# Kernel tuning notes

Measured on AMD Instinct MI355X. Metric: run time of the kernel, lower is better.

The kernel has to match this reference:

```python
import jax, jax.numpy as jnp
import numpy as np

N_NODES = 100000
N_EDGES = 1600000
IN_FEATS = 128
H_FEATS = 64
NEG_SLOPE = 0.2


def gat_layer(x, W, a_l, a_r, b, src, dst):
    # x: [N, Fin], W: [Fin, Fout], a_l/a_r/b: [Fout]
    h = x @ W                                   # [N, Fout]
    el = h @ a_l                                # [N]
    er = h @ a_r                                # [N]
    e = el[src] + er[dst]                       # [E]
    e = jnp.where(e > 0, e, NEG_SLOPE * e)      # leaky_relu
    # segment softmax over incoming edges of each dst node
    m = jax.ops.segment_max(e, dst, num_segments=N_NODES)   # [N], -inf for deg-0
    ex = jnp.exp(e - m[dst])                                 # [E]
    s = jax.ops.segment_sum(ex, dst, num_segments=N_NODES)   # [N]
    alpha = ex / s[dst]                                      # [E]
    out = jax.ops.segment_sum(alpha[:, None] * h[src], dst, num_segments=N_NODES)
    return jax.nn.relu(out + b)


def setup_inputs() -> dict:
    key = jax.random.key(0)
    ks = jax.random.split(key, 16)
    in_feat = jax.random.normal(ks[0], (N_NODES, IN_FEATS), dtype=jnp.float32)
    src = jax.random.randint(ks[1], (N_EDGES,), 0, N_NODES, dtype=jnp.int32)
    dst = jax.random.randint(ks[2], (N_EDGES,), 0, N_NODES, dtype=jnp.int32)
    def w(k, fin, fout):
        return jax.random.normal(k, (fin, fout), dtype=jnp.float32) * (1.0 / np.sqrt(fin))
    def v(k, f):
        return jax.random.normal(k, (f,), dtype=jnp.float32) * 0.1
    return {
        "in_feat": in_feat, "src": src, "dst": dst,
        "W1": w(ks[3], IN_FEATS, H_FEATS), "al1": v(ks[4], H_FEATS), "ar1": v(ks[5], H_FEATS), "b1": jnp.zeros((H_FEATS,), jnp.float32),
        "W2": w(ks[6], H_FEATS, H_FEATS), "al2": v(ks[7], H_FEATS), "ar2": v(ks[8], H_FEATS), "b2": jnp.zeros((H_FEATS,), jnp.float32),
        "W3": w(ks[9], H_FEATS, H_FEATS), "al3": v(ks[10], H_FEATS), "ar3": v(ks[11], H_FEATS), "b3": jnp.zeros((H_FEATS,), jnp.float32),
    }


def reference(in_feat, src, dst, W1, al1, ar1, b1, W2, al2, ar2, b2, W3, al3, ar3, b3):
    h = gat_layer(in_feat, W1, al1, ar1, b1, src, dst)
    h = gat_layer(h, W2, al2, ar2, b2, src, dst)
    h = gat_layer(h, W3, al3, ar3, b3, src, dst)
    return h
```

## Files before the change

### kernel.cpp

```cpp
#include <hip/hip_runtime.h>
#include <hip/hip_fp16.h>
#include <math.h>

#define HF 64
#define LEAKY 0.2f
#define NBLK 256
#define NPB 512
#define MAXNB 256

typedef _Float16 f16x2 __attribute__((ext_vector_type(2)));

__device__ __forceinline__ float dot2f(f16x2 a, f16x2 b, float c) {
#if __has_builtin(__builtin_amdgcn_fdot2)
    return __builtin_amdgcn_fdot2(a, b, c, false);
#else
    return fmaf((float)a[0], (float)b[0], fmaf((float)a[1], (float)b[1], c));
#endif
}


__global__ __launch_bounds__(256)
void part_count(const int* __restrict__ dst, int* __restrict__ Cmat, int E, int nb) {
    __shared__ int lc[MAXNB];
    int tid = threadIdx.x;
    for (int t = tid; t < nb; t += 256) lc[t] = 0;
    __syncthreads();
    int chunk = (E + NBLK - 1) / NBLK;
    int b0 = blockIdx.x * chunk, b1 = min(b0 + chunk, E);
    for (int i = b0 + tid; i < b1; i += 256)
        atomicAdd(&lc[dst[i] >> 9], 1);
    __syncthreads();
    for (int t = tid; t < nb; t += 256) Cmat[t * NBLK + blockIdx.x] = lc[t];
}

__global__ __launch_bounds__(256)
void scan_offsets(const int* __restrict__ Cmat, int* __restrict__ Omat,
                  int* __restrict__ bbase, int E, int nb) {
    __shared__ int tot[256];
    int t = threadIdx.x;
    int s = 0;
    if (t < nb)
        for (int blk = 0; blk < NBLK; ++blk) s += Cmat[t * NBLK + blk];
    tot[t] = s;
    __syncthreads();
    for (int off = 1; off < 256; off <<= 1) {
        int u = (t >= off) ? tot[t - off] : 0;
        __syncthreads();
        tot[t] += u;
        __syncthreads();
    }
    int excl = tot[t] - s;
    if (t < nb) {
        bbase[t] = excl;
        int run = excl;
        for (int blk = 0; blk < NBLK; ++blk) {
            Omat[t * NBLK + blk] = run;
            run += Cmat[t * NBLK + blk];
        }
    }
    if (t == 0) bbase[nb] = E;
}

__global__ __launch_bounds__(256)
void part_scatter(const int* __restrict__ src, const int* __restrict__ dst,
                  const int* __restrict__ Omat, int2* __restrict__ part, int E, int nb) {
    __shared__ int ocur[MAXNB];
    int tid = threadIdx.x;
    for (int t = tid; t < nb; t += 256) ocur[t] = Omat[t * NBLK + blockIdx.x];
    __syncthreads();
    int chunk = (E + NBLK - 1) / NBLK;
    int b0 = blockIdx.x * chunk, b1 = min(b0 + chunk, E);
    for (int i = b0 + tid; i < b1; i += 256) {
        int s = src[i], d = dst[i];
        int pos = atomicAdd(&ocur[d >> 9], 1);
        part[pos] = make_int2(s, d);
    }
}

__global__ __launch_bounds__(NPB)
void bucket_csr(const int2* __restrict__ part, const int* __restrict__ bbase,
                int* __restrict__ row_ptr, int* __restrict__ ssrc, int N, int E, int nb) {
    int b = blockIdx.x, tid = threadIdx.x;
    int bstart = bbase[b], bend = bbase[b + 1];
    int nb0 = b << 9;
    __shared__ int cnt[NPB];
    cnt[tid] = 0;
    __syncthreads();
    for (int i = bstart + tid; i < bend; i += NPB)
        atomicAdd(&cnt[part[i].y & (NPB - 1)], 1);
    __syncthreads();
    int v = cnt[tid];
    for (int off = 1; off < NPB; off <<= 1) {
        int u = (tid >= off) ? cnt[tid - off] : 0;
        __syncthreads();
        cnt[tid] += u;
        __syncthreads();
    }
    int excl = cnt[tid] - v;
    int node = nb0 + tid;
    if (node < N) row_ptr[node] = bstart + excl;
    __syncthreads();
    cnt[tid] = bstart + excl;
    __syncthreads();
    for (int i = bstart + tid; i < bend; i += NPB) {
        int2 e = part[i];
        int slot = atomicAdd(&cnt[e.y & (NPB - 1)], 1);
        ssrc[slot] = e.x;
    }
    if (b == nb - 1 && tid == 0) row_ptr[N] = E;
}


template <int K, bool XF16>
__global__ __launch_bounds__(256)
void gemm_kernel(const void* __restrict__ Xv, const float* __restrict__ W,
                 const float* __restrict__ al, const float* __restrict__ ar,
                 __half* __restrict__ H2, float* __restrict__ el, float* __restrict__ er,
                 int n, int ntiles) {
    constexpr int K2 = K / 2;
    constexpr int F4 = K / 4;
    constexpr int NL = 64 * F4 / 256;
    __shared__ f16x2 Wh[K2 * 64];
    __shared__ f16x2 Xh[2][64 * K2];
    int tid = threadIdx.x;

    int tpb = (ntiles + gridDim.x - 1) / gridDim.x;
    int t0 = blockIdx.x * tpb, t1 = min(t0 + tpb, ntiles);
    if (t0 >= t1) return;

    for (int idx = tid; idx < K2 * 64; idx += 256) {
        int k2 = idx >> 6, c = idx & 63;
        f16x2 h;
        h[0] = (_Float16)W[(2 * k2) * 64 + c];
        h[1] = (_Float16)W[(2 * k2 + 1) * 64 + c];
        Wh[idx] = h;
    }

    float4 xregf[XF16 ? 1 : NL];
    uint2 xregh[XF16 ? NL : 1];

    auto load_regs = [&](int t) {
        int rb = t * 64;
#pragma unroll
        for (int j = 0; j < NL; ++j) {
            int idx = tid + j * 256;
            int row = idx / F4;
            bool ok = rb + row < n;
            if constexpr (XF16) {
                uint2 z = make_uint2(0u, 0u);
                xregh[j] = ok ? ((const uint2*)Xv)[(size_t)rb * (K / 4) + idx] : z;
            } else {
                float4 z = make_float4(0.f, 0.f, 0.f, 0.f);
                xregf[j] = ok ? ((const float4*)Xv)[(size_t)rb * (K / 4) + idx] : z;
            }
        }
    };
    auto store_X = [&](int buf) {
#pragma unroll
        for (int j = 0; j < NL; ++j) {
            int idx = tid + j * 256;
            int row = idx / F4, k4 = idx % F4;
            int sw = (row & 15) << 1;
            f16x2 h0, h1;
            if constexpr (XF16) {
                h0 = *(f16x2*)&xregh[j].x;
                h1 = *(f16x2*)&xregh[j].y;
            } else {
                h0[0] = (_Float16)xregf[j].x; h0[1] = (_Float16)xregf[j].y;
                h1[0] = (_Float16)xregf[j].z; h1[1] = (_Float16)xregf[j].w;
            }
            Xh[buf][row * K2 + ((2 * k4) ^ sw)] = h0;
            Xh[buf][row * K2 + ((2 * k4 + 1) ^ sw)] = h1;
        }
    };

    int tc = tid & 15, tr = tid >> 4;
    float alv[4], arv[4];
#pragma unroll
    for (int i = 0; i < 4; ++i) { alv[i] = al[tc * 4 + i]; arv[i] = ar[tc * 4 + i]; }

    load_regs(t0);
    store_X(0);
    __syncthreads();
    int cur = 0;

    for (int t = t0; t < t1; ++t) {
        bool pf = (t + 1 < t1);
        if (pf) load_regs(t + 1);

        float acc[4][4] = {};
#pragma unroll 4
        for (int k2 = 0; k2 < K2; k2 += 2) {
            f16x2 xa[4], xb[4];
#pragma unroll
            for (int r = 0; r < 4; ++r) {
                int row = tr * 4 + r;
                int sw = (row & 15) << 1;
                const f16x2* p = &Xh[cur][row * K2 + (k2 ^ sw)];
                xa[r] = p[0];
                xb[r] = p[1];
            }
            const f16x2* w0 = &Wh[k2 * 64 + tc * 4];
            const f16x2* w1 = &Wh[(k2 + 1) * 64 + tc * 4];
#pragma unroll
            for (int i = 0; i < 4; ++i) {
                f16x2 wv0 = w0[i], wv1 = w1[i];
#pragma unroll
                for (int r = 0; r < 4; ++r) {
                    acc[r][i] = dot2f(xa[r], wv0, acc[r][i]);
                    acc[r][i] = dot2f(xb[r], wv1, acc[r][i]);
                }
            }
        }

        int r0 = t * 64 + tr * 4;
#pragma unroll
        for (int r = 0; r < 4; ++r) {
            if (r0 + r >= n) continue;
            __half2 h01 = __floats2half2_rn(acc[r][0], acc[r][1]);
            __half2 h23 = __floats2half2_rn(acc[r][2], acc[r][3]);
            uint2 u = make_uint2(*(unsigned*)&h01, *(unsigned*)&h23);
            ((uint2*)(H2 + (size_t)(r0 + r) * HF))[tc] = u;
            float pl = acc[r][0] * alv[0] + acc[r][1] * alv[1] + acc[r][2] * alv[2] + acc[r][3] * alv[3];
            float pr = acc[r][0] * arv[0] + acc[r][1] * arv[1] + acc[r][2] * arv[2] + acc[r][3] * arv[3];
#pragma unroll
            for (int off = 1; off < 16; off <<= 1) {
                pl += __shfl_xor(pl, off);
                pr += __shfl_xor(pr, off);
            }
            if (tc == 0) { el[r0 + r] = pl; er[r0 + r] = pr; }
        }

        if (pf) store_X(cur ^ 1);
        __syncthreads();
        if (pf) cur ^= 1;
    }
}

template <bool YF16>
__device__ __forceinline__
void node_fullwave(int node, const int* __restrict__ row_ptr, const int* __restrict__ ssrc,
                   const float* __restrict__ el, const float* __restrict__ er,
                   const uint2* __restrict__ H2v, const __half* __restrict__ H2,
                   float4 bv, const float* __restrict__ b, void* __restrict__ Y,
                   int lane, int g, int fl) {
    int s0 = row_ptr[node], s1 = row_ptr[node + 1];
    int d = s1 - s0;
    float ern = er[node];

    if (d <= 64) {
        int sidx = 0;
        float e = -INFINITY;
        if (lane < d) {
            sidx = ssrc[s0 + lane];
            e = el[sidx] + ern;
            e = e > 0.f ? e : LEAKY * e;
        }
        float m = e;
#pragma unroll
        for (int off = 32; off; off >>= 1) m = fmaxf(m, __shfl_xor(m, off));
        float p = (lane < d) ? __expf(e - m) : 0.f;
        float psum = p;
#pragma unroll
        for (int off = 32; off; off >>= 1) psum += __shfl_xor(psum, off);

        float4 acc = make_float4(0.f, 0.f, 0.f, 0.f);
        int nchunk = (d + 31) >> 5;
        for (int c = 0; c < nchunk; ++c) {
            int jb = c * 32 + g;
            int ss[8];
            float pp[8];
#pragma unroll
            for (int u = 0; u < 8; ++u) {
                ss[u] = __shfl(sidx, jb + 4 * u);
                pp[u] = __shfl(p, jb + 4 * u);
            }
            uint2 vv[8];
#pragma unroll
            for (int u = 0; u < 8; ++u) vv[u] = H2v[(size_t)ss[u] * 16 + fl];
#pragma unroll
            for (int u = 0; u < 8; ++u) {
                __half2 a = *(__half2*)&vv[u].x;
                __half2 b2 = *(__half2*)&vv[u].y;
                float2 fa = __half22float2(a);
                float2 fb = __half22float2(b2);
                acc.x = fmaf(pp[u], fa.x, acc.x);
                acc.y = fmaf(pp[u], fa.y, acc.y);
                acc.z = fmaf(pp[u], fb.x, acc.z);
                acc.w = fmaf(pp[u], fb.y, acc.w);
            }
        }
#pragma unroll
        for (int off = 16; off <= 32; off <<= 1) {
            acc.x += __shfl_xor(acc.x, off);
            acc.y += __shfl_xor(acc.y, off);
            acc.z += __shfl_xor(acc.z, off);
            acc.w += __shfl_xor(acc.w, off);
        }
        float inv = d ? 1.f / psum : 0.f;
        float4 o;
        o.x = fmaf(acc.x, inv, bv.x);
        o.y = fmaf(acc.y, inv, bv.y);
        o.z = fmaf(acc.z, inv, bv.z);
        o.w = fmaf(acc.w, inv, bv.w);
        o.x = o.x > 0.f ? o.x : 0.f;
        o.y = o.y > 0.f ? o.y : 0.f;
        o.z = o.z > 0.f ? o.z : 0.f;
        o.w = o.w > 0.f ? o.w : 0.f;
        if (g == 0) {
            if constexpr (YF16) {
                __half2 a = __floats2half2_rn(o.x, o.y);
                __half2 c = __floats2half2_rn(o.z, o.w);
                ((uint2*)Y)[(size_t)node * 16 + fl] = make_uint2(*(unsigned*)&a, *(unsigned*)&c);
            } else {
                ((float4*)Y)[(size_t)node * 16 + fl] = o;
            }
        }
    } else {
        float m = -INFINITY;
        for (int j = s0 + lane; j < s1; j += 64) {
            float e = el[ssrc[j]] + ern;
            e = e > 0.f ? e : LEAKY * e;
            m = fmaxf(m, e);
        }
#pragma unroll
        for (int off = 32; off; off >>= 1) m = fmaxf(m, __shfl_xor(m, off));
        float acc = 0.f, psum = 0.f;
        for (int j = s0; j < s1; ++j) {
            int s = ssrc[j];
            float e = el[s] + ern;
            e = e > 0.f ? e : LEAKY * e;
            float p = __expf(e - m);
            psum += p;
            acc = fmaf(p, __half2float(H2[(size_t)s * HF + lane]), acc);
        }
        float o = acc / psum + b[lane];
        o = o > 0.f ? o : 0.f;
        if constexpr (YF16)
            ((__half*)Y)[(size_t)node * HF + lane] = __float2half(o);
        else
            ((float*)Y)[(size_t)node * HF + lane] = o;
    }
}

template <bool YF16>
__global__ __launch_bounds__(256)
void edge_kernel(const int* __restrict__ row_ptr, const int* __restrict__ ssrc,
                 const float* __restrict__ el, const float* __restrict__ er,
                 const __half* __restrict__ H2, const float* __restrict__ b,
                 void* __restrict__ Y, int n) {
    int wave = threadIdx.x >> 6, lane = threadIdx.x & 63;
    int half = lane >> 5, hl = lane & 31;
    int g = lane >> 4, fl = lane & 15;
    const uint2* H2v = (const uint2*)H2;
    float4 bv = ((const float4*)b)[fl];
    int npairs = (n + 1) >> 1;

    for (int pr = blockIdx.x * 4 + wave; pr < npairs; pr += gridDim.x * 4) {
        int nodeA = pr * 2;
        int myNode = nodeA + half;
        bool ok = myNode < n;
        int s0 = 0, d = 0;
        if (ok) {
            s0 = row_ptr[myNode];
            d = row_ptr[myNode + 1] - s0;
        }
        int dA = __shfl(d, 0), dB = __shfl(d, 32);

        if (dA <= 32 && dB <= 32) {
            float ern = ok ? er[myNode] : 0.f;
            int sidx = 0;
            float e = -INFINITY;
            if (hl < d) {
                sidx = ssrc[s0 + hl];
                e = el[sidx] + ern;
                e = e > 0.f ? e : LEAKY * e;
            }
            float m = e;
#pragma unroll
            for (int off = 16; off; off >>= 1) m = fmaxf(m, __shfl_xor(m, off));
            float p = (hl < d) ? __expf(e - m) : 0.f;
            float psum = p;
#pragma unroll
            for (int off = 16; off; off >>= 1) psum += __shfl_xor(psum, off);

            float4 acc = make_float4(0.f, 0.f, 0.f, 0.f);
            int dg = (g >> 1) ? dB : dA;
            int hbase = (g >> 1) << 5;
            int gpar = g & 1;
            int nch = (dg + 15) >> 4;
            for (int c = 0; c < nch; ++c) {
                int ss[8];
                float pp[8];
#pragma unroll
                for (int u = 0; u < 8; ++u) {
                    int sl = hbase + c * 16 + 2 * u + gpar;
                    ss[u] = __shfl(sidx, sl);
                    pp[u] = __shfl(p, sl);
                }
                uint2 vv[8];
#pragma unroll
                for (int u = 0; u < 8; ++u) vv[u] = H2v[(size_t)ss[u] * 16 + fl];
#pragma unroll
                for (int u = 0; u < 8; ++u) {
                    __half2 a = *(__half2*)&vv[u].x;
                    __half2 b2 = *(__half2*)&vv[u].y;
                    float2 fa = __half22float2(a);
                    float2 fb = __half22float2(b2);
                    acc.x = fmaf(pp[u], fa.x, acc.x);
                    acc.y = fmaf(pp[u], fa.y, acc.y);
                    acc.z = fmaf(pp[u], fb.x, acc.z);
                    acc.w = fmaf(pp[u], fb.y, acc.w);
                }
            }
            acc.x += __shfl_xor(acc.x, 16);
            acc.y += __shfl_xor(acc.y, 16);
            acc.z += __shfl_xor(acc.z, 16);
            acc.w += __shfl_xor(acc.w, 16);
            float inv = d ? 1.f / psum : 0.f;
            float4 o;
            o.x = fmaf(acc.x, inv, bv.x);
            o.y = fmaf(acc.y, inv, bv.y);
            o.z = fmaf(acc.z, inv, bv.z);
            o.w = fmaf(acc.w, inv, bv.w);
            o.x = o.x > 0.f ? o.x : 0.f;
            o.y = o.y > 0.f ? o.y : 0.f;
            o.z = o.z > 0.f ? o.z : 0.f;
            o.w = o.w > 0.f ? o.w : 0.f;
            if (!(g & 1) && ok) {
                if constexpr (YF16) {
                    __half2 a = __floats2half2_rn(o.x, o.y);
                    __half2 c2 = __floats2half2_rn(o.z, o.w);
                    ((uint2*)Y)[(size_t)myNode * 16 + fl] = make_uint2(*(unsigned*)&a, *(unsigned*)&c2);
                } else {
                    ((float4*)Y)[(size_t)myNode * 16 + fl] = o;
                }
            }
        } else {
            node_fullwave<YF16>(nodeA, row_ptr, ssrc, el, er, H2v, H2, bv, b, Y, lane, g, fl);
            if (nodeA + 1 < n)
                node_fullwave<YF16>(nodeA + 1, row_ptr, ssrc, el, er, H2v, H2, bv, b, Y, lane, g, fl);
        }
    }
}


extern "C" void kernel_launch(void* const* d_in, const int* in_sizes, int n_in,
                              void* d_out, int out_size, void* d_ws, size_t ws_size,
                              hipStream_t stream) {
    const int N = in_sizes[0] / 128;
    const int E = in_sizes[1];
    const int nb = (N + NPB - 1) >> 9;

    const float* in_feat = (const float*)d_in[0];
    const int* src = (const int*)d_in[1];
    const int* dst = (const int*)d_in[2];
    const float* W1 = (const float*)d_in[3];
    const float* al1 = (const float*)d_in[4];
    const float* ar1 = (const float*)d_in[5];
    const float* b1 = (const float*)d_in[6];
    const float* W2 = (const float*)d_in[7];
    const float* al2 = (const float*)d_in[8];
    const float* ar2 = (const float*)d_in[9];
    const float* b2 = (const float*)d_in[10];
    const float* W3 = (const float*)d_in[11];
    const float* al3 = (const float*)d_in[12];
    const float* ar3 = (const float*)d_in[13];
    const float* b3 = (const float*)d_in[14];

    char* ws = (char*)d_ws;
    size_t off = 0;
    auto alloc = [&](size_t bytes) {
        void* p = ws + off;
        off += (bytes + 255) & ~(size_t)255;
        return p;
    };
    int* row_ptr = (int*)alloc(((size_t)N + 1) * 4);
    int* ssrc = (int*)alloc((size_t)E * 4);
    int2* part = (int2*)alloc((size_t)E * 8);
    int* Cmat = (int*)alloc((size_t)MAXNB * NBLK * 4);
    int* Omat = (int*)alloc((size_t)MAXNB * NBLK * 4);
    int* bbase = (int*)alloc(((size_t)MAXNB + 1) * 4);
    float* el = (float*)alloc((size_t)N * 4);
    float* er = (float*)alloc((size_t)N * 4);
    __half* H2buf = (__half*)alloc((size_t)N * HF * 2);
    __half* Y2buf = (__half*)alloc((size_t)N * HF * 2);

    part_count<<<NBLK, 256, 0, stream>>>(dst, Cmat, E, nb);
    scan_offsets<<<1, 256, 0, stream>>>(Cmat, Omat, bbase, E, nb);
    part_scatter<<<NBLK, 256, 0, stream>>>(src, dst, Omat, part, E, nb);
    bucket_csr<<<nb, NPB, 0, stream>>>(part, bbase, row_ptr, ssrc, N, E, nb);

    int ntiles = (N + 63) / 64;
    int gg = (ntiles + 2) / 3;
    int ge = 2048;

    gemm_kernel<128, false><<<gg, 256, 0, stream>>>(in_feat, W1, al1, ar1, H2buf, el, er, N, ntiles);
    edge_kernel<true><<<ge, 256, 0, stream>>>(row_ptr, ssrc, el, er, H2buf, b1, Y2buf, N);
    gemm_kernel<64, true><<<gg, 256, 0, stream>>>(Y2buf, W2, al2, ar2, H2buf, el, er, N, ntiles);
    edge_kernel<true><<<ge, 256, 0, stream>>>(row_ptr, ssrc, el, er, H2buf, b2, Y2buf, N);
    gemm_kernel<64, true><<<gg, 256, 0, stream>>>(Y2buf, W3, al3, ar3, H2buf, el, er, N, ntiles);
    edge_kernel<false><<<ge, 256, 0, stream>>>(row_ptr, ssrc, el, er, H2buf, b3, d_out, N);
}
```

Before: 281.1 us.

## Replace LDS-tiled dot2 GEMM with per-wave MFMA 16x16x32 f16 kernel

Rewrites the node-feature GEMM to use MFMA 16x16x32 f16 instructions. Each wave processes 16-row slabs, loads A fragments straight from global memory into registers, and keeps the W fragments resident in registers. This removes the shared-memory double buffering, the block barriers and the scalar fdot2 loop. The cost is uncoalesced per-row fragment loads, scattered 2-byte H stores, and a fixed grid of 512 blocks.

```diff
diff --git a/kernel.cpp b/kernel.cpp
--- a/kernel.cpp
+++ b/kernel.cpp
@@ -8,15 +8,9 @@
 #define NPB 512
 #define MAXNB 256
 
-typedef _Float16 f16x2 __attribute__((ext_vector_type(2)));
-
-__device__ __forceinline__ float dot2f(f16x2 a, f16x2 b, float c) {
-#if __has_builtin(__builtin_amdgcn_fdot2)
-    return __builtin_amdgcn_fdot2(a, b, c, false);
-#else
-    return fmaf((float)a[0], (float)b[0], fmaf((float)a[1], (float)b[1], c));
-#endif
-}
+typedef _Float16 half4_t __attribute__((ext_vector_type(4)));
+typedef _Float16 half8_t __attribute__((ext_vector_type(8)));
+typedef float floatx4 __attribute__((ext_vector_type(4)));
 
 
 __global__ __launch_bounds__(256)
@@ -112,128 +106,97 @@
 
 
 template <int K, bool XF16>
-__global__ __launch_bounds__(256)
-void gemm_kernel(const void* __restrict__ Xv, const float* __restrict__ W,
-                 const float* __restrict__ al, const float* __restrict__ ar,
-                 __half* __restrict__ H2, float* __restrict__ el, float* __restrict__ er,
-                 int n, int ntiles) {
-    constexpr int K2 = K / 2;
-    constexpr int F4 = K / 4;
-    constexpr int NL = 64 * F4 / 256;
-    __shared__ f16x2 Wh[K2 * 64];
-    __shared__ f16x2 Xh[2][64 * K2];
-    int tid = threadIdx.x;
-
-    int tpb = (ntiles + gridDim.x - 1) / gridDim.x;
-    int t0 = blockIdx.x * tpb, t1 = min(t0 + tpb, ntiles);
-    if (t0 >= t1) return;
-
-    for (int idx = tid; idx < K2 * 64; idx += 256) {
-        int k2 = idx >> 6, c = idx & 63;
-        f16x2 h;
-        h[0] = (_Float16)W[(2 * k2) * 64 + c];
-        h[1] = (_Float16)W[(2 * k2 + 1) * 64 + c];
-        Wh[idx] = h;
-    }
-
-    float4 xregf[XF16 ? 1 : NL];
-    uint2 xregh[XF16 ? NL : 1];
-
-    auto load_regs = [&](int t) {
-        int rb = t * 64;
-#pragma unroll
-        for (int j = 0; j < NL; ++j) {
-            int idx = tid + j * 256;
-            int row = idx / F4;
-            bool ok = rb + row < n;
+__global__ __launch_bounds__(256, 3)
+void gemm_mfma(const void* __restrict__ Xv, const float* __restrict__ W,
+               const float* __restrict__ al, const float* __restrict__ ar,
+               __half* __restrict__ H2, float* __restrict__ el, float* __restrict__ er,
+               int n, int nslabs) {
+    constexpr int KS = K / 32;
+    int lane = threadIdx.x & 63;
+    int li = lane & 15, g = lane >> 4;
+    int wid = blockIdx.x * 4 + (threadIdx.x >> 6);
+    int wstride = gridDim.x * 4;
+
+    half8_t bf[4][KS];
+    float alv[4], arv[4];
+#pragma unroll
+    for (int ct = 0; ct < 4; ++ct) {
+        int col = ct * 16 + li;
+        alv[ct] = al[col];
+        arv[ct] = ar[col];
+#pragma unroll
+        for (int ks = 0; ks < KS; ++ks) {
+            half8_t b;
+#pragma unroll
+            for (int j = 0; j < 4; ++j) {
+                b[j]     = (_Float16)W[(ks * 32 + 4 * g + j) * 64 + col];
+                b[4 + j] = (_Float16)W[(ks * 32 + 16 + 4 * g + j) * 64 + col];
+            }
+            bf[ct][ks] = b;
+        }
+    }
+
+    for (int s = wid; s < nslabs; s += wstride) {
+        int row = s * 16 + li;
+        int rc = row < n ? row : n - 1;
+
+        half8_t a[KS];
+#pragma unroll
+        for (int ks = 0; ks < KS; ++ks) {
             if constexpr (XF16) {
-                uint2 z = make_uint2(0u, 0u);
-                xregh[j] = ok ? ((const uint2*)Xv)[(size_t)rb * (K / 4) + idx] : z;
+                const __half* Xh = (const __half*)Xv;
+                half4_t h0 = *(const half4_t*)(Xh + (size_t)rc * K + ks * 32 + 4 * g);
+                half4_t h1 = *(const half4_t*)(Xh + (size_t)rc * K + ks * 32 + 16 + 4 * g);
+                half8_t av;
+#pragma unroll
+                for (int j = 0; j < 4; ++j) { av[j] = h0[j]; av[4 + j] = h1[j]; }
+                a[ks] = av;
             } else {
-                float4 z = make_float4(0.f, 0.f, 0.f, 0.f);
-                xregf[j] = ok ? ((const float4*)Xv)[(size_t)rb * (K / 4) + idx] : z;
-            }
-        }
-    };
-    auto store_X = [&](int buf) {
-#pragma unroll
-        for (int j = 0; j < NL; ++j) {
-            int idx = tid + j * 256;
-            int row = idx / F4, k4 = idx % F4;
-            int sw = (row & 15) << 1;
-            f16x2 h0, h1;
-            if constexpr (XF16) {
-                h0 = *(f16x2*)&xregh[j].x;
-                h1 = *(f16x2*)&xregh[j].y;
-            } else {
-                h0[0] = (_Float16)xregf[j].x; h0[1] = (_Float16)xregf[j].y;
-                h1[0] = (_Float16)xregf[j].z; h1[1] = (_Float16)xregf[j].w;
-            }
-            Xh[buf][row * K2 + ((2 * k4) ^ sw)] = h0;
-            Xh[buf][row * K2 + ((2 * k4 + 1) ^ sw)] = h1;
-        }
-    };
-
-    int tc = tid & 15, tr = tid >> 4;
-    float alv[4], arv[4];
-#pragma unroll
-    for (int i = 0; i < 4; ++i) { alv[i] = al[tc * 4 + i]; arv[i] = ar[tc * 4 + i]; }
-
-    load_regs(t0);
-    store_X(0);
-    __syncthreads();
-    int cur = 0;
-
-    for (int t = t0; t < t1; ++t) {
-        bool pf = (t + 1 < t1);
-        if (pf) load_regs(t + 1);
-
-        float acc[4][4] = {};
-#pragma unroll 4
-        for (int k2 = 0; k2 < K2; k2 += 2) {
-            f16x2 xa[4], xb[4];
-#pragma unroll
-            for (int r = 0; r < 4; ++r) {
-                int row = tr * 4 + r;
-                int sw = (row & 15) << 1;
-                const f16x2* p = &Xh[cur][row * K2 + (k2 ^ sw)];
-                xa[r] = p[0];
-                xb[r] = p[1];
-            }
-            const f16x2* w0 = &Wh[k2 * 64 + tc * 4];
-            const f16x2* w1 = &Wh[(k2 + 1) * 64 + tc * 4];
-#pragma unroll
-            for (int i = 0; i < 4; ++i) {
-                f16x2 wv0 = w0[i], wv1 = w1[i];
-#pragma unroll
-                for (int r = 0; r < 4; ++r) {
-                    acc[r][i] = dot2f(xa[r], wv0, acc[r][i]);
-                    acc[r][i] = dot2f(xb[r], wv1, acc[r][i]);
-                }
-            }
-        }
-
-        int r0 = t * 64 + tr * 4;
+                const float* Xf = (const float*)Xv;
+                float4 v0 = *(const float4*)(Xf + (size_t)rc * K + ks * 32 + 4 * g);
+                float4 v1 = *(const float4*)(Xf + (size_t)rc * K + ks * 32 + 16 + 4 * g);
+                half8_t av;
+                av[0] = (_Float16)v0.x; av[1] = (_Float16)v0.y;
+                av[2] = (_Float16)v0.z; av[3] = (_Float16)v0.w;
+                av[4] = (_Float16)v1.x; av[5] = (_Float16)v1.y;
+                av[6] = (_Float16)v1.z; av[7] = (_Float16)v1.w;
+                a[ks] = av;
+            }
+        }
+
+        floatx4 acc[4];
+#pragma unroll
+        for (int ct = 0; ct < 4; ++ct) acc[ct] = (floatx4){0.f, 0.f, 0.f, 0.f};
+#pragma unroll
+        for (int ks = 0; ks < KS; ++ks)
+#pragma unroll
+            for (int ct = 0; ct < 4; ++ct)
+                acc[ct] = __builtin_amdgcn_mfma_f32_16x16x32_f16(a[ks], bf[ct][ks], acc[ct], 0, 0, 0);
+
+        float pl[4], pr[4];
 #pragma unroll
         for (int r = 0; r < 4; ++r) {
-            if (r0 + r >= n) continue;
-            __half2 h01 = __floats2half2_rn(acc[r][0], acc[r][1]);
-            __half2 h23 = __floats2half2_rn(acc[r][2], acc[r][3]);
-            uint2 u = make_uint2(*(unsigned*)&h01, *(unsigned*)&h23);
-            ((uint2*)(H2 + (size_t)(r0 + r) * HF))[tc] = u;
-            float pl = acc[r][0] * alv[0] + acc[r][1] * alv[1] + acc[r][2] * alv[2] + acc[r][3] * alv[3];
-            float pr = acc[r][0] * arv[0] + acc[r][1] * arv[1] + acc[r][2] * arv[2] + acc[r][3] * arv[3];
+            pl[r] = acc[0][r] * alv[0] + acc[1][r] * alv[1] + acc[2][r] * alv[2] + acc[3][r] * alv[3];
+            pr[r] = acc[0][r] * arv[0] + acc[1][r] * arv[1] + acc[2][r] * arv[2] + acc[3][r] * arv[3];
+        }
+#pragma unroll
+        for (int r = 0; r < 4; ++r)
 #pragma unroll
             for (int off = 1; off < 16; off <<= 1) {
-                pl += __shfl_xor(pl, off);
-                pr += __shfl_xor(pr, off);
-            }
-            if (tc == 0) { el[r0 + r] = pl; er[r0 + r] = pr; }
-        }
-
-        if (pf) store_X(cur ^ 1);
-        __syncthreads();
-        if (pf) cur ^= 1;
+                pl[r] += __shfl_xor(pl[r], off);
+                pr[r] += __shfl_xor(pr[r], off);
+            }
+        int rowbase = s * 16 + 4 * g;
+#pragma unroll
+        for (int r = 0; r < 4; ++r) {
+            int ro = rowbase + r;
+            if (ro < n) {
+#pragma unroll
+                for (int ct = 0; ct < 4; ++ct)
+                    H2[(size_t)ro * HF + ct * 16 + li] = __float2half(acc[ct][r]);
+                if (li == 0) { el[ro] = pl[r]; er[ro] = pr[r]; }
+            }
+        }
     }
 }
 
@@ -491,14 +454,14 @@
     part_scatter<<<NBLK, 256, 0, stream>>>(src, dst, Omat, part, E, nb);
     bucket_csr<<<nb, NPB, 0, stream>>>(part, bbase, row_ptr, ssrc, N, E, nb);
 
-    int ntiles = (N + 63) / 64;
-    int gg = (ntiles + 2) / 3;
+    int nslabs = (N + 15) / 16;
+    int gg = 512;
     int ge = 2048;
 
-    gemm_kernel<128, false><<<gg, 256, 0, stream>>>(in_feat, W1, al1, ar1, H2buf, el, er, N, ntiles);
+    gemm_mfma<128, false><<<gg, 256, 0, stream>>>(in_feat, W1, al1, ar1, H2buf, el, er, N, nslabs);
     edge_kernel<true><<<ge, 256, 0, stream>>>(row_ptr, ssrc, el, er, H2buf, b1, Y2buf, N);
-    gemm_kernel<64, true><<<gg, 256, 0, stream>>>(Y2buf, W2, al2, ar2, H2buf, el, er, N, ntiles);
+    gemm_mfma<64, true><<<gg, 256, 0, stream>>>(Y2buf, W2, al2, ar2, H2buf, el, er, N, nslabs);
     edge_kernel<true><<<ge, 256, 0, stream>>>(row_ptr, ssrc, el, er, H2buf, b2, Y2buf, N);
-    gemm_kernel<64, true><<<gg, 256, 0, stream>>>(Y2buf, W3, al3, ar3, H2buf, el, er, N, ntiles);
+    gemm_mfma<64, true><<<gg, 256, 0, stream>>>(Y2buf, W3, al3, ar3, H2buf, el, er, N, nslabs);
     edge_kernel<false><<<ge, 256, 0, stream>>>(row_ptr, ssrc, el, er, H2buf, b3, d_out, N);
 }
```

Result: faster. 228.3 us (-18.8%).
